# Performance work log

Measured on AMD Instinct MI355X. Metric: run time of the kernel, lower is better.

## Reference

```python
import jax, jax.numpy as jnp
import numpy as np

B, N = 8, 50000
DIM, C_DIM, TASK_DIM, H, NB, OUT = 3, 64, 512, 64, 5, 12


def setup_inputs() -> dict:
    key = jax.random.key(0)
    ks = jax.random.split(key, 16)
    s = lambda fan_in: 1.0 / np.sqrt(fan_in)
    inp = {
        "p": jax.random.normal(ks[0], (B, N, DIM), dtype=jnp.float32),
        "c": jax.random.normal(ks[1], (B, N, C_DIM), dtype=jnp.float32),
        "task_feature": jax.random.normal(ks[2], (B, TASK_DIM), dtype=jnp.float32),
        # params (stored as [in, out] so y = x @ W + b)
        "fc_p_W": jax.random.uniform(ks[3], (DIM, H), jnp.float32, -s(DIM), s(DIM)),
        "fc_p_b": jax.random.uniform(ks[4], (H,), jnp.float32, -s(DIM), s(DIM)),
        "fc_c_W": jax.random.uniform(ks[5], (NB, C_DIM + TASK_DIM, H), jnp.float32, -s(C_DIM + TASK_DIM), s(C_DIM + TASK_DIM)),
        "fc_c_b": jax.random.uniform(ks[6], (NB, H), jnp.float32, -s(C_DIM + TASK_DIM), s(C_DIM + TASK_DIM)),
        "blk0_W": jax.random.uniform(ks[7], (NB, H, H), jnp.float32, -s(H), s(H)),
        "blk0_b": jax.random.uniform(ks[8], (NB, H), jnp.float32, -s(H), s(H)),
        "blk1_W": jax.random.uniform(ks[9], (NB, H, H), jnp.float32, -s(H), s(H)) * 0.1,
        "blk1_b": jax.random.uniform(ks[10], (NB, H), jnp.float32, -s(H), s(H)),
        "fc_out_W": jax.random.uniform(ks[11], (H, OUT), jnp.float32, -s(H), s(H)),
        "fc_out_b": jax.random.uniform(ks[12], (OUT,), jnp.float32, -s(H), s(H)),
    }
    return inp


def reference(p, c, task_feature, fc_p_W, fc_p_b, fc_c_W, fc_c_b,
              blk0_W, blk0_b, blk1_W, blk1_b, fc_out_W, fc_out_b):
    b, n = p.shape[0], p.shape[1]
    # expand task feature to every point and concat with point-wise code c
    tf = jnp.broadcast_to(task_feature[:, None, :], (b, n, task_feature.shape[-1]))
    cc = jnp.concatenate([c, tf], axis=-1)              # [B, N, 576]
    net = p @ fc_p_W + fc_p_b                           # [B, N, H]
    for i in range(fc_c_W.shape[0]):
        net = net + cc @ fc_c_W[i] + fc_c_b[i]          # conditioning
        # ResnetBlockFC: dx = fc_1(relu(fc_0(relu(x)))); out = x + dx
        h = jax.nn.relu(net) @ blk0_W[i] + blk0_b[i]
        dx = jax.nn.relu(h) @ blk1_W[i] + blk1_b[i]
        net = net + dx
    out = jax.nn.relu(net) @ fc_out_W + fc_out_b        # [B, N, 12]
    return out
```

## Files before the change

kernel.cpp:

```cpp
#include <hip/hip_runtime.h>

#define B_    8
#define N_    50000
#define NB_   5
#define OUT_  12
#define TILES_ 4
#define TILES_PER_BATCH 3125
#define BLOCKS_PER_BATCH 782

typedef _Float16 half8 __attribute__((ext_vector_type(8)));
typedef float   floatx4 __attribute__((ext_vector_type(4)));

__device__ __forceinline__ half8 ldg8(const _Float16* p) {
    union { uint4 u; half8 h; } x;
    x.u = *(const uint4*)p;
    return x.h;
}

__device__ __forceinline__ half8 packB(floatx4 a, floatx4 b) {
    half8 r;
    r[0] = (_Float16)fmaxf(a[0], 0.f); r[1] = (_Float16)fmaxf(a[1], 0.f);
    r[2] = (_Float16)fmaxf(a[2], 0.f); r[3] = (_Float16)fmaxf(a[3], 0.f);
    r[4] = (_Float16)fmaxf(b[0], 0.f); r[5] = (_Float16)fmaxf(b[1], 0.f);
    r[6] = (_Float16)fmaxf(b[2], 0.f); r[7] = (_Float16)fmaxf(b[3], 0.f);
    return r;
}

__device__ __forceinline__ void load8(half8 (&A)[8], const _Float16* base, int q16m) {
    #pragma unroll
    for (int T = 0; T < 4; ++T)
        #pragma unroll
        for (int h = 0; h < 2; ++h)
            A[T * 2 + h] = ldg8(base + (size_t)(T * 128 + h * 64 + q16m) * 8);
}

__global__ void prep_kernel(const float* __restrict__ fc_c_W,
                            const float* __restrict__ blk0_W,
                            const float* __restrict__ blk1_W,
                            const float* __restrict__ fc_out_W,
                            const float* __restrict__ tf,
                            _Float16* __restrict__ ws_w,
                            _Float16* __restrict__ ws_fco,
                            float* __restrict__ partials, int R) {
    int bid = blockIdx.x, tid = threadIdx.x;
    if (bid < 32) {
        int u = bid * 256 + tid;
        if (u < 7680) {
            int m15 = u & 15, q = (u >> 4) & 3, h = (u >> 6) & 1, T = (u >> 7) & 3;
            int mi = u >> 9;
            int mat = mi / 5, i = mi % 5;
            int n = T * 16 + m15;
            _Float16 out[8];
            #pragma unroll
            for (int j = 0; j < 8; ++j) {
                float v;
                if (mat == 0) {
                    int k = 32 * h + 8 * q + j;
                    v = fc_c_W[((size_t)i * 576 + k) * 64 + n];
                } else {
                    int f = 32 * h + 16 * (j >> 2) + 4 * q + (j & 3);
                    const float* W = (mat == 1) ? blk0_W : blk1_W;
                    v = W[((size_t)i * 64 + f) * 64 + n];
                }
                out[j] = (_Float16)v;
            }
            uint4 val = *(uint4*)out;
            for (int r = 0; r < R; ++r)
                *(uint4*)(ws_w + (size_t)r * 61440 + (size_t)u * 8) = val;
        } else {
            int e = u - 7680;
            _Float16 out[8] = {};
            if (e < 128) {
                int m15 = e & 15, q = (e >> 4) & 3, h = (e >> 6) & 1;
                #pragma unroll
                for (int j = 0; j < 8; ++j) {
                    int f = 32 * h + 16 * (j >> 2) + 4 * q + (j & 3);
                    out[j] = (m15 < OUT_) ? (_Float16)fc_out_W[f * OUT_ + m15] : (_Float16)0.f;
                }
            }
            uint4 val = *(uint4*)out;
            for (int r = 0; r < R; ++r)
                *(uint4*)(ws_fco + (size_t)r * 4096 + (size_t)e * 8) = val;
        }
    } else {
        int idx2 = bid - 32;
        int b = idx2 / 10, rem = idx2 % 10, i = rem >> 1, hf = rem & 1;
        int g = tid >> 6, j = tid & 63;
        const float* W  = fc_c_W + ((size_t)i * 576 + 64) * 64;
        const float* tb = tf + b * 512;
        int t0 = hf * 256 + g * 64;
        float acc = 0.f;
        #pragma unroll 8
        for (int t = 0; t < 64; ++t)
            acc += tb[t0 + t] * W[(size_t)(t0 + t) * 64 + j];
        partials[(((b * 5 + i) << 3) + (hf * 4 + g)) * 64 + j] = acc;
    }
}

__global__ void finalize_tp(const float* __restrict__ partials,
                            const float* __restrict__ fc_c_b,
                            const float* __restrict__ fc_p_b,
                            float* __restrict__ tp) {
    int u = blockIdx.x * 256 + threadIdx.x;
    if (u >= 2560) return;
    int b = u / 320, rem = u % 320, i = rem >> 6, j = rem & 63;
    float s = fc_c_b[i * 64 + j] + ((i == 0) ? fc_p_b[j] : 0.f);
    #pragma unroll
    for (int k = 0; k < 8; ++k)
        s += partials[(((b * 5 + i) << 3) + k) * 64 + j];
    tp[u] = s;
}

__device__ __forceinline__ void resblock(
    half8 (&Ac)[8], half8 (&Ab)[8],
    floatx4 (&net4)[TILES_][4], const half8 (&cB)[TILES_][2],
    int tc, int i, int q, int q16m,
    const float* __restrict__ tp_b, const float* __restrict__ b0g,
    const float* __restrict__ b1g, const _Float16* __restrict__ wsr,
    const _Float16* __restrict__ next_cond_base, bool last)
{
    floatx4 tpv[4], bb0[4], bb1[4];
    #pragma unroll
    for (int T = 0; T < 4; ++T) {
        int off = i * 64 + 16 * T + 4 * q;
        tpv[T] = *(const floatx4*)(tp_b + off);
        bb0[T] = *(const floatx4*)(b0g + off);
        bb1[T] = *(const floatx4*)(b1g + off);
    }
    #pragma unroll
    for (int t = 0; t < TILES_; ++t) {
        if (t >= tc) break;
        #pragma unroll
        for (int T = 0; T < 4; ++T) {
            floatx4 a = net4[t][T];
            a = __builtin_amdgcn_mfma_f32_16x16x32_f16(Ac[2 * T], cB[t][0], a, 0, 0, 0);
            a = __builtin_amdgcn_mfma_f32_16x16x32_f16(Ac[2 * T + 1], cB[t][1], a, 0, 0, 0);
            net4[t][T] = a + tpv[T];
        }
    }
    load8(Ac, wsr + (size_t)(10 + i) * 4096, q16m);
    #pragma unroll
    for (int t = 0; t < TILES_; ++t) {
        if (t >= tc) break;
        half8 Bn0 = packB(net4[t][0], net4[t][1]);
        half8 Bn1 = packB(net4[t][2], net4[t][3]);
        floatx4 hh[4];
        #pragma unroll
        for (int T = 0; T < 4; ++T) {
            floatx4 a = bb0[T];
            a = __builtin_amdgcn_mfma_f32_16x16x32_f16(Ab[2 * T], Bn0, a, 0, 0, 0);
            a = __builtin_amdgcn_mfma_f32_16x16x32_f16(Ab[2 * T + 1], Bn1, a, 0, 0, 0);
            hh[T] = a;
        }
        half8 Bh0 = packB(hh[0], hh[1]);
        half8 Bh1 = packB(hh[2], hh[3]);
        #pragma unroll
        for (int T = 0; T < 4; ++T) {
            floatx4 a = bb1[T];
            a = __builtin_amdgcn_mfma_f32_16x16x32_f16(Ac[2 * T], Bh0, a, 0, 0, 0);
            a = __builtin_amdgcn_mfma_f32_16x16x32_f16(Ac[2 * T + 1], Bh1, a, 0, 0, 0);
            net4[t][T] += a;
        }
    }
    load8(Ab, next_cond_base, q16m);
    if (!last)
        load8(Ac, wsr + (size_t)(5 + i + 1) * 4096, q16m);
}

__global__ __launch_bounds__(64, 2) void decoder_kernel(
    const float* __restrict__ p_g, const float* __restrict__ c_g,
    const float* __restrict__ blk0_b, const float* __restrict__ blk1_b,
    const float* __restrict__ fc_p_W, const float* __restrict__ fc_out_b,
    const _Float16* __restrict__ ws_w, const _Float16* __restrict__ ws_fco,
    const float* __restrict__ tp_g, float* __restrict__ out_g, int rmask)
{
    const int bid   = blockIdx.x;
    const int batch = bid / BLOCKS_PER_BATCH;
    const int blk   = bid % BLOCKS_PER_BATCH;
    const int tile0 = blk * TILES_;
    const int tc    = min(TILES_, TILES_PER_BATCH - tile0);
    const long gbase = (long)batch * N_ + (long)tile0 * 16;
    const int lane = threadIdx.x;
    const int q = lane >> 4, m15 = lane & 15;
    const int q16m = q * 16 + m15;
    const _Float16* wsr  = ws_w  + (size_t)(bid & rmask) * 61440;
    const _Float16* fcor = ws_fco + (size_t)(bid & rmask) * 4096;
    const float* tp_b = tp_g + batch * (NB_ * 64);

    half8 X[8], Y[8];
    load8(X, wsr, q16m);
    load8(Y, wsr + (size_t)5 * 4096, q16m);

    half8 cB[TILES_][2];
    #pragma unroll
    for (int t = 0; t < TILES_; ++t) {
        if (t >= tc) break;
        const float* cr = c_g + (size_t)(gbase + t * 16 + m15) * 64;
        #pragma unroll
        for (int h = 0; h < 2; ++h) {
            float4 v0 = *(const float4*)(cr + 32 * h + 8 * q);
            float4 v1 = *(const float4*)(cr + 32 * h + 8 * q + 4);
            half8 r;
            r[0] = (_Float16)v0.x; r[1] = (_Float16)v0.y;
            r[2] = (_Float16)v0.z; r[3] = (_Float16)v0.w;
            r[4] = (_Float16)v1.x; r[5] = (_Float16)v1.y;
            r[6] = (_Float16)v1.z; r[7] = (_Float16)v1.w;
            cB[t][h] = r;
        }
    }

    floatx4 fw[3][4];
    #pragma unroll
    for (int d = 0; d < 3; ++d)
        #pragma unroll
        for (int T = 0; T < 4; ++T)
            fw[d][T] = *(const floatx4*)(fc_p_W + d * 64 + 16 * T + 4 * q);
    floatx4 net4[TILES_][4];
    #pragma unroll
    for (int t = 0; t < TILES_; ++t) {
        if (t >= tc) break;
        long g = gbase + t * 16 + m15;
        float pp0 = p_g[g * 3 + 0], pp1 = p_g[g * 3 + 1], pp2 = p_g[g * 3 + 2];
        #pragma unroll
        for (int T = 0; T < 4; ++T)
            net4[t][T] = fw[0][T] * pp0 + fw[1][T] * pp1 + fw[2][T] * pp2;
    }

    resblock(X, Y, net4, cB, tc, 0, q, q16m, tp_b, blk0_b, blk1_b, wsr, wsr + (size_t)1 * 4096, false);
    resblock(Y, X, net4, cB, tc, 1, q, q16m, tp_b, blk0_b, blk1_b, wsr, wsr + (size_t)2 * 4096, false);
    resblock(X, Y, net4, cB, tc, 2, q, q16m, tp_b, blk0_b, blk1_b, wsr, wsr + (size_t)3 * 4096, false);
    resblock(Y, X, net4, cB, tc, 3, q, q16m, tp_b, blk0_b, blk1_b, wsr, wsr + (size_t)4 * 4096, false);
    resblock(X, Y, net4, cB, tc, 4, q, q16m, tp_b, blk0_b, blk1_b, wsr, fcor, true);

    floatx4 ob = {0.f, 0.f, 0.f, 0.f};
    if (q < 3) ob = *(const floatx4*)(fc_out_b + 4 * q);
    #pragma unroll
    for (int t = 0; t < TILES_; ++t) {
        if (t >= tc) break;
        half8 Bn0 = packB(net4[t][0], net4[t][1]);
        half8 Bn1 = packB(net4[t][2], net4[t][3]);
        floatx4 a = ob;
        a = __builtin_amdgcn_mfma_f32_16x16x32_f16(Y[0], Bn0, a, 0, 0, 0);
        a = __builtin_amdgcn_mfma_f32_16x16x32_f16(Y[1], Bn1, a, 0, 0, 0);
        if (q < 3) {
            long g = gbase + t * 16 + m15;
            *(float4*)(out_g + g * OUT_ + 4 * q) = make_float4(a[0], a[1], a[2], a[3]);
        }
    }
}

extern "C" void kernel_launch(void* const* d_in, const int* in_sizes, int n_in,
                              void* d_out, int out_size, void* d_ws, size_t ws_size,
                              hipStream_t stream) {
    const float* p        = (const float*)d_in[0];
    const float* c        = (const float*)d_in[1];
    const float* tf       = (const float*)d_in[2];
    const float* fc_p_W   = (const float*)d_in[3];
    const float* fc_p_b   = (const float*)d_in[4];
    const float* fc_c_W   = (const float*)d_in[5];
    const float* fc_c_b   = (const float*)d_in[6];
    const float* blk0_W   = (const float*)d_in[7];
    const float* blk0_b   = (const float*)d_in[8];
    const float* blk1_W   = (const float*)d_in[9];
    const float* blk1_b   = (const float*)d_in[10];
    const float* fc_out_W = (const float*)d_in[11];
    const float* fc_out_b = (const float*)d_in[12];
    float* out = (float*)d_out;

    int R = 8;
    while (R > 1 && ((size_t)R * (61440 + 4096) * 2 + 81920 + 10240) > ws_size) R >>= 1;

    _Float16* ws_w   = (_Float16*)d_ws;
    _Float16* ws_fco = ws_w + (size_t)R * 61440;
    float* partials  = (float*)(ws_fco + (size_t)R * 4096);
    float* tp        = partials + 20480;

    prep_kernel<<<112, 256, 0, stream>>>(fc_c_W, blk0_W, blk1_W, fc_out_W, tf,
                                         ws_w, ws_fco, partials, R);
    finalize_tp<<<10, 256, 0, stream>>>(partials, fc_c_b, fc_p_b, tp);
    decoder_kernel<<<B_ * BLOCKS_PER_BATCH, 64, 0, stream>>>(
        p, c, blk0_b, blk1_b, fc_p_W, fc_out_b, ws_w, ws_fco, tp, out, R - 1);
}
```

Measured before the change: 237.3 us.

## Stage weights in LDS with persistent 512-thread blocks and fold blk1 bias

The decoder now launches 768 blocks of 8 waves. Each block first copies all fp16 weights, the per-batch conditioning terms, the biases and fc_p_W into about 134 KB of LDS. Weight fragments are then read from LDS instead of from global memory through R replicated copies. Work is flattened across batches into groups of 4 tiles, with a few waves taking a second pass, and the blk1 bias is folded into the next block's conditioning term via finalize_tp. The pack conversions use cvt_pkrtz. The trade-off is one block per CU and a prologue copy in every block, which limits overlap of global loads.

Result: slower. 705.4 us (+197.3%).

```diff
diff --git a/kernel.cpp b/kernel.cpp
--- a/kernel.cpp
+++ b/kernel.cpp
@@ -4,34 +4,46 @@
 #define N_    50000
 #define NB_   5
 #define OUT_  12
+#define THREADS 512
+#define GRID   768
 #define TILES_ 4
-#define TILES_PER_BATCH 3125
-#define BLOCKS_PER_BATCH 782
-
-typedef _Float16 half8 __attribute__((ext_vector_type(8)));
+#define NGROUPS 6250
+#define PRIMARY 6144
+#define EXTRA  (NGROUPS - PRIMARY)
+
+#define WL_OFF   0
+#define TPL_OFF  124928
+#define B0L_OFF  135168
+#define B14_OFF  136448
+#define FPW_OFF  136704
+#define SMEM_BYTES 137472
+
+typedef _Float16 half8  __attribute__((ext_vector_type(8)));
+typedef __fp16   fp16x2 __attribute__((ext_vector_type(2)));
 typedef float   floatx4 __attribute__((ext_vector_type(4)));
 
-__device__ __forceinline__ half8 ldg8(const _Float16* p) {
+__device__ __forceinline__ half8 ldl8(const _Float16* p) {
     union { uint4 u; half8 h; } x;
     x.u = *(const uint4*)p;
     return x.h;
 }
 
 __device__ __forceinline__ half8 packB(floatx4 a, floatx4 b) {
-    half8 r;
-    r[0] = (_Float16)fmaxf(a[0], 0.f); r[1] = (_Float16)fmaxf(a[1], 0.f);
-    r[2] = (_Float16)fmaxf(a[2], 0.f); r[3] = (_Float16)fmaxf(a[3], 0.f);
-    r[4] = (_Float16)fmaxf(b[0], 0.f); r[5] = (_Float16)fmaxf(b[1], 0.f);
-    r[6] = (_Float16)fmaxf(b[2], 0.f); r[7] = (_Float16)fmaxf(b[3], 0.f);
-    return r;
-}
-
-__device__ __forceinline__ void load8(half8 (&A)[8], const _Float16* base, int q16m) {
+    union { fp16x2 h2[4]; half8 h8; } u;
+    u.h2[0] = __builtin_amdgcn_cvt_pkrtz(fmaxf(a[0], 0.f), fmaxf(a[1], 0.f));
+    u.h2[1] = __builtin_amdgcn_cvt_pkrtz(fmaxf(a[2], 0.f), fmaxf(a[3], 0.f));
+    u.h2[2] = __builtin_amdgcn_cvt_pkrtz(fmaxf(b[0], 0.f), fmaxf(b[1], 0.f));
+    u.h2[3] = __builtin_amdgcn_cvt_pkrtz(fmaxf(b[2], 0.f), fmaxf(b[3], 0.f));
+    return u.h8;
+}
+
+__device__ __forceinline__ void loadL8(half8 (&A)[8], const _Float16* wl, int stage, int lane) {
+    const _Float16* b = wl + (size_t)stage * 512 * 8;
     #pragma unroll
     for (int T = 0; T < 4; ++T)
         #pragma unroll
         for (int h = 0; h < 2; ++h)
-            A[T * 2 + h] = ldg8(base + (size_t)(T * 128 + h * 64 + q16m) * 8);
+            A[2 * T + h] = ldl8(b + (size_t)(T * 128 + h * 64 + lane) * 8);
 }
 
 __global__ void prep_kernel(const float* __restrict__ fc_c_W,
@@ -40,8 +52,7 @@
                             const float* __restrict__ fc_out_W,
                             const float* __restrict__ tf,
                             _Float16* __restrict__ ws_w,
-                            _Float16* __restrict__ ws_fco,
-                            float* __restrict__ partials, int R) {
+                            float* __restrict__ partials) {
     int bid = blockIdx.x, tid = threadIdx.x;
     if (bid < 32) {
         int u = bid * 256 + tid;
@@ -64,9 +75,7 @@
                 }
                 out[j] = (_Float16)v;
             }
-            uint4 val = *(uint4*)out;
-            for (int r = 0; r < R; ++r)
-                *(uint4*)(ws_w + (size_t)r * 61440 + (size_t)u * 8) = val;
+            *(uint4*)(ws_w + (size_t)u * 8) = *(uint4*)out;
         } else {
             int e = u - 7680;
             _Float16 out[8] = {};
@@ -78,9 +87,7 @@
                     out[j] = (m15 < OUT_) ? (_Float16)fc_out_W[f * OUT_ + m15] : (_Float16)0.f;
                 }
             }
-            uint4 val = *(uint4*)out;
-            for (int r = 0; r < R; ++r)
-                *(uint4*)(ws_fco + (size_t)r * 4096 + (size_t)e * 8) = val;
+            *(uint4*)(ws_w + (size_t)u * 8) = *(uint4*)out;
         }
     } else {
         int idx2 = bid - 32;
@@ -100,48 +107,41 @@
 __global__ void finalize_tp(const float* __restrict__ partials,
                             const float* __restrict__ fc_c_b,
                             const float* __restrict__ fc_p_b,
+                            const float* __restrict__ blk1_b,
                             float* __restrict__ tp) {
     int u = blockIdx.x * 256 + threadIdx.x;
     if (u >= 2560) return;
     int b = u / 320, rem = u % 320, i = rem >> 6, j = rem & 63;
-    float s = fc_c_b[i * 64 + j] + ((i == 0) ? fc_p_b[j] : 0.f);
+    float s = fc_c_b[i * 64 + j] + ((i == 0) ? fc_p_b[j] : blk1_b[(i - 1) * 64 + j]);
     #pragma unroll
     for (int k = 0; k < 8; ++k)
         s += partials[(((b * 5 + i) << 3) + k) * 64 + j];
     tp[u] = s;
 }
 
-__device__ __forceinline__ void resblock(
-    half8 (&Ac)[8], half8 (&Ab)[8],
-    floatx4 (&net4)[TILES_][4], const half8 (&cB)[TILES_][2],
-    int tc, int i, int q, int q16m,
-    const float* __restrict__ tp_b, const float* __restrict__ b0g,
-    const float* __restrict__ b1g, const _Float16* __restrict__ wsr,
-    const _Float16* __restrict__ next_cond_base, bool last)
+__device__ __forceinline__ void rb(half8 (&Ac)[8], half8 (&Ab)[8],
+    floatx4 (&net4)[TILES_][4], const half8 (&cB)[TILES_][2], const int (&bt)[TILES_],
+    int i, int q, int lane, const _Float16* wl, const float* tp_l, const float* b0_l,
+    int next_stage, bool last)
 {
-    floatx4 tpv[4], bb0[4], bb1[4];
-    #pragma unroll
-    for (int T = 0; T < 4; ++T) {
-        int off = i * 64 + 16 * T + 4 * q;
-        tpv[T] = *(const floatx4*)(tp_b + off);
-        bb0[T] = *(const floatx4*)(b0g + off);
-        bb1[T] = *(const floatx4*)(b1g + off);
-    }
+    floatx4 bb0[4];
+    #pragma unroll
+    for (int T = 0; T < 4; ++T)
+        bb0[T] = *(const floatx4*)(b0_l + i * 64 + 16 * T + 4 * q);
     #pragma unroll
     for (int t = 0; t < TILES_; ++t) {
-        if (t >= tc) break;
+        const float* tpb = tp_l + (bt[t] * NB_ + i) * 64 + 4 * q;
         #pragma unroll
         for (int T = 0; T < 4; ++T) {
             floatx4 a = net4[t][T];
             a = __builtin_amdgcn_mfma_f32_16x16x32_f16(Ac[2 * T], cB[t][0], a, 0, 0, 0);
             a = __builtin_amdgcn_mfma_f32_16x16x32_f16(Ac[2 * T + 1], cB[t][1], a, 0, 0, 0);
-            net4[t][T] = a + tpv[T];
-        }
-    }
-    load8(Ac, wsr + (size_t)(10 + i) * 4096, q16m);
+            net4[t][T] = a + *(const floatx4*)(tpb + 16 * T);
+        }
+    }
+    loadL8(Ac, wl, 10 + i, lane);
     #pragma unroll
     for (int t = 0; t < TILES_; ++t) {
-        if (t >= tc) break;
         half8 Bn0 = packB(net4[t][0], net4[t][1]);
         half8 Bn1 = packB(net4[t][2], net4[t][3]);
         floatx4 hh[4];
@@ -156,95 +156,133 @@
         half8 Bh1 = packB(hh[2], hh[3]);
         #pragma unroll
         for (int T = 0; T < 4; ++T) {
-            floatx4 a = bb1[T];
+            floatx4 a = net4[t][T];
             a = __builtin_amdgcn_mfma_f32_16x16x32_f16(Ac[2 * T], Bh0, a, 0, 0, 0);
             a = __builtin_amdgcn_mfma_f32_16x16x32_f16(Ac[2 * T + 1], Bh1, a, 0, 0, 0);
-            net4[t][T] += a;
-        }
-    }
-    load8(Ab, next_cond_base, q16m);
+            net4[t][T] = a;
+        }
+    }
+    loadL8(Ab, wl, next_stage, lane);
     if (!last)
-        load8(Ac, wsr + (size_t)(5 + i + 1) * 4096, q16m);
-}
-
-__global__ __launch_bounds__(64, 2) void decoder_kernel(
+        loadL8(Ac, wl, 5 + i + 1, lane);
+}
+
+__global__ __launch_bounds__(THREADS, 1) void decoder_kernel(
     const float* __restrict__ p_g, const float* __restrict__ c_g,
     const float* __restrict__ blk0_b, const float* __restrict__ blk1_b,
     const float* __restrict__ fc_p_W, const float* __restrict__ fc_out_b,
-    const _Float16* __restrict__ ws_w, const _Float16* __restrict__ ws_fco,
-    const float* __restrict__ tp_g, float* __restrict__ out_g, int rmask)
+    const _Float16* __restrict__ ws_w, const float* __restrict__ tp_g,
+    float* __restrict__ out_g)
 {
-    const int bid   = blockIdx.x;
-    const int batch = bid / BLOCKS_PER_BATCH;
-    const int blk   = bid % BLOCKS_PER_BATCH;
-    const int tile0 = blk * TILES_;
-    const int tc    = min(TILES_, TILES_PER_BATCH - tile0);
-    const long gbase = (long)batch * N_ + (long)tile0 * 16;
-    const int lane = threadIdx.x;
-    const int q = lane >> 4, m15 = lane & 15;
-    const int q16m = q * 16 + m15;
-    const _Float16* wsr  = ws_w  + (size_t)(bid & rmask) * 61440;
-    const _Float16* fcor = ws_fco + (size_t)(bid & rmask) * 4096;
-    const float* tp_b = tp_g + batch * (NB_ * 64);
-
-    half8 X[8], Y[8];
-    load8(X, wsr, q16m);
-    load8(Y, wsr + (size_t)5 * 4096, q16m);
-
-    half8 cB[TILES_][2];
-    #pragma unroll
-    for (int t = 0; t < TILES_; ++t) {
-        if (t >= tc) break;
-        const float* cr = c_g + (size_t)(gbase + t * 16 + m15) * 64;
-        #pragma unroll
-        for (int h = 0; h < 2; ++h) {
-            float4 v0 = *(const float4*)(cr + 32 * h + 8 * q);
-            float4 v1 = *(const float4*)(cr + 32 * h + 8 * q + 4);
-            half8 r;
-            r[0] = (_Float16)v0.x; r[1] = (_Float16)v0.y;
-            r[2] = (_Float16)v0.z; r[3] = (_Float16)v0.w;
-            r[4] = (_Float16)v1.x; r[5] = (_Float16)v1.y;
-            r[6] = (_Float16)v1.z; r[7] = (_Float16)v1.w;
-            cB[t][h] = r;
-        }
-    }
-
-    floatx4 fw[3][4];
-    #pragma unroll
-    for (int d = 0; d < 3; ++d)
-        #pragma unroll
-        for (int T = 0; T < 4; ++T)
-            fw[d][T] = *(const floatx4*)(fc_p_W + d * 64 + 16 * T + 4 * q);
-    floatx4 net4[TILES_][4];
-    #pragma unroll
-    for (int t = 0; t < TILES_; ++t) {
-        if (t >= tc) break;
-        long g = gbase + t * 16 + m15;
-        float pp0 = p_g[g * 3 + 0], pp1 = p_g[g * 3 + 1], pp2 = p_g[g * 3 + 2];
-        #pragma unroll
-        for (int T = 0; T < 4; ++T)
-            net4[t][T] = fw[0][T] * pp0 + fw[1][T] * pp1 + fw[2][T] * pp2;
-    }
-
-    resblock(X, Y, net4, cB, tc, 0, q, q16m, tp_b, blk0_b, blk1_b, wsr, wsr + (size_t)1 * 4096, false);
-    resblock(Y, X, net4, cB, tc, 1, q, q16m, tp_b, blk0_b, blk1_b, wsr, wsr + (size_t)2 * 4096, false);
-    resblock(X, Y, net4, cB, tc, 2, q, q16m, tp_b, blk0_b, blk1_b, wsr, wsr + (size_t)3 * 4096, false);
-    resblock(Y, X, net4, cB, tc, 3, q, q16m, tp_b, blk0_b, blk1_b, wsr, wsr + (size_t)4 * 4096, false);
-    resblock(X, Y, net4, cB, tc, 4, q, q16m, tp_b, blk0_b, blk1_b, wsr, fcor, true);
+    extern __shared__ char smem[];
+    _Float16* wl   = (_Float16*)(smem + WL_OFF);
+    float*    tp_l = (float*)(smem + TPL_OFF);
+    float*    b0_l = (float*)(smem + B0L_OFF);
+    float*    b14_l= (float*)(smem + B14_OFF);
+    float*    fpw_l= (float*)(smem + FPW_OFF);
+
+    const int tid = threadIdx.x, bid = blockIdx.x;
+
+    {
+        uint4* dw = (uint4*)wl;
+        const uint4* sw = (const uint4*)ws_w;
+        for (int u = tid; u < 7808; u += THREADS) dw[u] = sw[u];
+        uint4* dt = (uint4*)tp_l;  const uint4* st = (const uint4*)tp_g;
+        for (int u = tid; u < 640; u += THREADS) dt[u] = st[u];
+        uint4* db = (uint4*)b0_l;  const uint4* sb = (const uint4*)blk0_b;
+        for (int u = tid; u < 80; u += THREADS) db[u] = sb[u];
+        uint4* d4 = (uint4*)b14_l; const uint4* s4 = (const uint4*)(blk1_b + 4 * 64);
+        if (tid < 16) d4[tid] = s4[tid];
+        uint4* df = (uint4*)fpw_l; const uint4* sf = (const uint4*)fc_p_W;
+        if (tid < 48) df[tid] = sf[tid];
+    }
+    __syncthreads();
+
+    const int lane = tid & 63;
+    const int wv   = tid >> 6;
+    const int q    = lane >> 4;
+    const int m15  = lane & 15;
+
+    int g_primary = (bid * 8 + wv) * TILES_;
+    int npass = 1, g_second = 0;
+    if ((bid % 7) == 0) {
+        int e = bid / 7;
+        if (e < EXTRA && wv == (e & 7)) { npass = 2; g_second = (PRIMARY + e) * TILES_; }
+    }
 
     floatx4 ob = {0.f, 0.f, 0.f, 0.f};
     if (q < 3) ob = *(const floatx4*)(fc_out_b + 4 * q);
-    #pragma unroll
-    for (int t = 0; t < TILES_; ++t) {
-        if (t >= tc) break;
-        half8 Bn0 = packB(net4[t][0], net4[t][1]);
-        half8 Bn1 = packB(net4[t][2], net4[t][3]);
-        floatx4 a = ob;
-        a = __builtin_amdgcn_mfma_f32_16x16x32_f16(Y[0], Bn0, a, 0, 0, 0);
-        a = __builtin_amdgcn_mfma_f32_16x16x32_f16(Y[1], Bn1, a, 0, 0, 0);
-        if (q < 3) {
-            long g = gbase + t * 16 + m15;
-            *(float4*)(out_g + g * OUT_ + 4 * q) = make_float4(a[0], a[1], a[2], a[3]);
+
+    #pragma unroll 1
+    for (int pass = 0; pass < npass; ++pass) {
+        int g0 = pass ? g_second : g_primary;
+        int bt[TILES_];
+        long pbase[TILES_];
+        #pragma unroll
+        for (int t = 0; t < TILES_; ++t) {
+            int gt = g0 + t;
+            int b  = gt / 3125;
+            int lt = gt - b * 3125;
+            bt[t] = b;
+            pbase[t] = (long)b * N_ + (long)lt * 16;
+        }
+
+        half8 X[8], Y[8];
+        loadL8(X, wl, 0, lane);
+        loadL8(Y, wl, 5, lane);
+
+        half8 cB[TILES_][2];
+        #pragma unroll
+        for (int t = 0; t < TILES_; ++t) {
+            const float* cr = c_g + (size_t)(pbase[t] + m15) * 64;
+            #pragma unroll
+            for (int h = 0; h < 2; ++h) {
+                float4 v0 = *(const float4*)(cr + 32 * h + 8 * q);
+                float4 v1 = *(const float4*)(cr + 32 * h + 8 * q + 4);
+                union { fp16x2 h2[4]; half8 h8; } u;
+                u.h2[0] = __builtin_amdgcn_cvt_pkrtz(v0.x, v0.y);
+                u.h2[1] = __builtin_amdgcn_cvt_pkrtz(v0.z, v0.w);
+                u.h2[2] = __builtin_amdgcn_cvt_pkrtz(v1.x, v1.y);
+                u.h2[3] = __builtin_amdgcn_cvt_pkrtz(v1.z, v1.w);
+                cB[t][h] = u.h8;
+            }
+        }
+
+        floatx4 net4[TILES_][4];
+        #pragma unroll
+        for (int t = 0; t < TILES_; ++t) {
+            long g = pbase[t] + m15;
+            float pp0 = p_g[g * 3 + 0], pp1 = p_g[g * 3 + 1], pp2 = p_g[g * 3 + 2];
+            #pragma unroll
+            for (int T = 0; T < 4; ++T) {
+                floatx4 w0 = *(const floatx4*)(fpw_l + 16 * T + 4 * q);
+                floatx4 w1 = *(const floatx4*)(fpw_l + 64 + 16 * T + 4 * q);
+                floatx4 w2 = *(const floatx4*)(fpw_l + 128 + 16 * T + 4 * q);
+                net4[t][T] = w0 * pp0 + w1 * pp1 + w2 * pp2;
+            }
+        }
+
+        rb(X, Y, net4, cB, bt, 0, q, lane, wl, tp_l, b0_l, 1, false);
+        rb(Y, X, net4, cB, bt, 1, q, lane, wl, tp_l, b0_l, 2, false);
+        rb(X, Y, net4, cB, bt, 2, q, lane, wl, tp_l, b0_l, 3, false);
+        rb(Y, X, net4, cB, bt, 3, q, lane, wl, tp_l, b0_l, 4, false);
+        rb(X, Y, net4, cB, bt, 4, q, lane, wl, tp_l, b0_l, 15, true);
+
+        floatx4 b14v[4];
+        #pragma unroll
+        for (int T = 0; T < 4; ++T)
+            b14v[T] = *(const floatx4*)(b14_l + 16 * T + 4 * q);
+        #pragma unroll
+        for (int t = 0; t < TILES_; ++t) {
+            half8 Bn0 = packB(net4[t][0] + b14v[0], net4[t][1] + b14v[1]);
+            half8 Bn1 = packB(net4[t][2] + b14v[2], net4[t][3] + b14v[3]);
+            floatx4 a = ob;
+            a = __builtin_amdgcn_mfma_f32_16x16x32_f16(Y[0], Bn0, a, 0, 0, 0);
+            a = __builtin_amdgcn_mfma_f32_16x16x32_f16(Y[1], Bn1, a, 0, 0, 0);
+            if (q < 3) {
+                long g = pbase[t] + m15;
+                *(float4*)(out_g + g * OUT_ + 4 * q) = make_float4(a[0], a[1], a[2], a[3]);
+            }
         }
     }
 }
@@ -267,17 +305,15 @@
     const float* fc_out_b = (const float*)d_in[12];
     float* out = (float*)d_out;
 
-    int R = 8;
-    while (R > 1 && ((size_t)R * (61440 + 4096) * 2 + 81920 + 10240) > ws_size) R >>= 1;
-
-    _Float16* ws_w   = (_Float16*)d_ws;
-    _Float16* ws_fco = ws_w + (size_t)R * 61440;
-    float* partials  = (float*)(ws_fco + (size_t)R * 4096);
-    float* tp        = partials + 20480;
-
-    prep_kernel<<<112, 256, 0, stream>>>(fc_c_W, blk0_W, blk1_W, fc_out_W, tf,
-                                         ws_w, ws_fco, partials, R);
-    finalize_tp<<<10, 256, 0, stream>>>(partials, fc_c_b, fc_p_b, tp);
-    decoder_kernel<<<B_ * BLOCKS_PER_BATCH, 64, 0, stream>>>(
-        p, c, blk0_b, blk1_b, fc_p_W, fc_out_b, ws_w, ws_fco, tp, out, R - 1);
-}
+    _Float16* ws_w  = (_Float16*)d_ws;
+    float* partials = (float*)((char*)d_ws + 131072);
+    float* tp       = (float*)((char*)d_ws + 131072 + 81920);
+
+    prep_kernel<<<112, 256, 0, stream>>>(fc_c_W, blk0_W, blk1_W, fc_out_W, tf, ws_w, partials);
+    finalize_tp<<<10, 256, 0, stream>>>(partials, fc_c_b, fc_p_b, blk1_b, tp);
+
+    (void)hipFuncSetAttribute((const void*)decoder_kernel,
+                        hipFuncAttributeMaxDynamicSharedMemorySize, SMEM_BYTES);
+    decoder_kernel<<<GRID, THREADS, SMEM_BYTES, stream>>>(
+        p, c, blk0_b, blk1_b, fc_p_W, fc_out_b, ws_w, tp, out);
+}
```
